# Kernel optimization log

Measured on AMD Instinct MI355X. Metric: run time of the kernel, lower is better.

The kernel has to match this reference:

```python
import jax, jax.numpy as jnp
import numpy as np

B, S, H = 2, 2048, 2048
NQ, NKV = 32, 8
HD = H // NQ  # 64


def setup_inputs() -> dict:
    key = jax.random.key(0)
    ks = jax.random.split(key, 9)
    s = 1.0 / np.sqrt(H)
    return {
        "x": jax.random.normal(ks[0], (B, S, H), dtype=jnp.float32),
        "Wq": jax.random.normal(ks[1], (H, H), dtype=jnp.float32) * s,
        "bq": jnp.zeros((H,), dtype=jnp.float32),
        "Wk": jax.random.normal(ks[2], (H, NKV * HD), dtype=jnp.float32) * s,
        "bk": jnp.zeros((NKV * HD,), dtype=jnp.float32),
        "Wv": jax.random.normal(ks[3], (H, NKV * HD), dtype=jnp.float32) * s,
        "bv": jnp.zeros((NKV * HD,), dtype=jnp.float32),
        "Wo": jax.random.normal(ks[4], (H, H), dtype=jnp.float32) * s,
        "bo": jnp.zeros((H,), dtype=jnp.float32),
    }


def reference(x, Wq, bq, Wk, bk, Wv, bv, Wo, bo):
    Bx, Sx, _ = x.shape
    g = NQ // NKV  # queries per kv head
    q = (x @ Wq + bq).reshape(Bx, Sx, NKV, g, HD)   # grouped query heads
    k = (x @ Wk + bk).reshape(Bx, Sx, NKV, HD)
    v = (x @ Wv + bv).reshape(Bx, Sx, NKV, HD)
    # scores: [B, NKV, g, S, S] -- broadcast KV across group instead of jnp.repeat
    scores = jnp.einsum('bshgd,bkhd->bhgsk', q, k) / jnp.sqrt(jnp.float32(HD))
    probs = jax.nn.softmax(scores, axis=-1)
    out = jnp.einsum('bhgsk,bkhd->bshgd', probs, v).reshape(Bx, Sx, H)
    return out @ Wo + bo
```

## Files before the change

### kernel.cpp

```cpp
#include <hip/hip_runtime.h>
#include <cstdint>
#include <cstddef>

typedef unsigned short u16;
typedef __bf16 bf16x8 __attribute__((ext_vector_type(8)));
typedef float f32x4 __attribute__((ext_vector_type(4)));
typedef unsigned short u16x4 __attribute__((ext_vector_type(4)));
typedef unsigned short u16x8 __attribute__((ext_vector_type(8)));
typedef uint32_t u32x4 __attribute__((ext_vector_type(4)));
typedef __attribute__((address_space(1))) unsigned int as1_uint;
typedef __attribute__((address_space(3))) unsigned int as3_uint;

__device__ __forceinline__ u16 f2bf(float f) {
  uint32_t u = __builtin_bit_cast(uint32_t, f);
  u += 0x7FFFu + ((u >> 16) & 1u);
  return (u16)(u >> 16);
}

__device__ __forceinline__ uint32_t cvtpk2bf(float a, float b) {
  uint32_t r;
  asm("v_cvt_pk_bf16_f32 %0, %1, %2" : "=v"(r) : "v"(a), "v"(b));
  return r;
}

__device__ __forceinline__ float max3f(float a, float b, float c) {
  return fmaxf(fmaxf(a, b), c);
}

__device__ __forceinline__ void gld_lds16(const void* g, void* l) {
  __builtin_amdgcn_global_load_lds((as1_uint*)g, (as3_uint*)l, 16, 0, 0);
}

__global__ __launch_bounds__(256) void k_cast(const float* __restrict__ in,
                                              u16* __restrict__ out, int n8) {
  int i = blockIdx.x * 256 + threadIdx.x;
  if (i >= n8) return;
  const float4* p = reinterpret_cast<const float4*>(in) + (size_t)i * 2;
  float4 a = p[0], b = p[1];
  u16x8 r;
  r[0] = f2bf(a.x); r[1] = f2bf(a.y); r[2] = f2bf(a.z); r[3] = f2bf(a.w);
  r[4] = f2bf(b.x); r[5] = f2bf(b.y); r[6] = f2bf(b.z); r[7] = f2bf(b.w);
  *reinterpret_cast<u16x8*>(out + (size_t)i * 8) = r;
}

__global__ __launch_bounds__(256) void k_transpose_all(const float* __restrict__ Wq,
                                                       const float* __restrict__ Wk,
                                                       const float* __restrict__ Wv,
                                                       const float* __restrict__ Wo,
                                                       u16* __restrict__ wqkvT,
                                                       u16* __restrict__ woT) {
  constexpr int K = 2048;
  const int z = blockIdx.z;
  const float* W; u16* Wt; int N;
  if (z == 0)      { W = Wq; Wt = wqkvT;                        N = 2048; }
  else if (z == 1) { W = Wo; Wt = woT;                          N = 2048; }
  else if (z == 2) { W = Wk; Wt = wqkvT + (size_t)2048 * 2048;  N = 512;  }
  else             { W = Wv; Wt = wqkvT + (size_t)2560 * 2048;  N = 512;  }
  const int n0 = blockIdx.x * 64;
  if (n0 >= N) return;
  __shared__ u16 tile[64][72];
  const int k0 = blockIdx.y * 64;
  const int r = threadIdx.x >> 4;
  const int c4 = (threadIdx.x & 15) * 4;
#pragma unroll
  for (int i = 0; i < 4; ++i) {
    int kk = r + i * 16;
    float4 v = *reinterpret_cast<const float4*>(W + (size_t)(k0 + kk) * N + n0 + c4);
    tile[kk][c4 + 0] = f2bf(v.x); tile[kk][c4 + 1] = f2bf(v.y);
    tile[kk][c4 + 2] = f2bf(v.z); tile[kk][c4 + 3] = f2bf(v.w);
  }
  __syncthreads();
#pragma unroll
  for (int i = 0; i < 4; ++i) {
    int nn = r + i * 16;
    u16x4 o;
    o[0] = tile[c4 + 0][nn]; o[1] = tile[c4 + 1][nn];
    o[2] = tile[c4 + 2][nn]; o[3] = tile[c4 + 3][nn];
    *reinterpret_cast<u16x4*>(Wt + (size_t)(n0 + nn) * K + k0 + c4) = o;
  }
}

__global__ __launch_bounds__(256) void k_transpose_v(const u16* __restrict__ qkv,
                                                     u16* __restrict__ vt) {
  __shared__ u16 tile[64][72];
  const int t0 = blockIdx.x * 64, kvh = blockIdx.y, b = blockIdx.z;
  const u16* src = qkv + ((size_t)(b * 2048) + t0) * 3072 + 2560 + kvh * 64;
  u16* dst = vt + ((size_t)(b * 8 + kvh) * 64) * 2048 + t0;
  const int r = threadIdx.x >> 3;
  const int c8 = (threadIdx.x & 7) * 8;
#pragma unroll
  for (int i = 0; i < 2; ++i) {
    int rr = r + i * 32;
    u16x8 v = *reinterpret_cast<const u16x8*>(src + (size_t)rr * 3072 + c8);
#pragma unroll
    for (int j = 0; j < 8; ++j) tile[c8 + j][rr] = v[j];
  }
  __syncthreads();
#pragma unroll
  for (int i = 0; i < 2; ++i) {
    int rr = r + i * 32;
    u16x8 o;
#pragma unroll
    for (int j = 0; j < 8; ++j) o[j] = tile[rr][c8 + j];
    *reinterpret_cast<u16x8*>(dst + (size_t)rr * 2048 + c8) = o;
  }
}

template <bool F32OUT>
__global__ __launch_bounds__(256) void k_gemm(const u16* __restrict__ A,
                                              const u16* __restrict__ Bt,
                                              const float* __restrict__ b0,
                                              const float* __restrict__ b1,
                                              const float* __restrict__ b2,
                                              void* __restrict__ Cout,
                                              int M, int N, int K,
                                              int n1, int n2,
                                              int scaleN, float scaleV) {
  __shared__ __align__(16) u16 As[128 * 64];
  __shared__ __align__(16) u16 Bs[128 * 64];
  const int id = blockIdx.y * gridDim.x + blockIdx.x;
  const int cpx = (gridDim.x * gridDim.y) >> 3;
  const int nid = (id & 7) * cpx + (id >> 3);
  const int m0 = (nid / gridDim.x) * 128, n0 = (nid % gridDim.x) * 128;
  const int tid = threadIdx.x;
  const int l = tid & 63, w = tid >> 6;
  const int wm = w >> 1, wn = w & 1;
  const int lr = l & 15, lo = l >> 4;
  const int srow = w * 8 + (l >> 3);
  const int sc = (l & 7) ^ ((l >> 3) & 7);
  f32x4 acc[4][4] = {};
  for (int kt = 0; kt < K; kt += 64) {
    __syncthreads();
#pragma unroll
    for (int it = 0; it < 4; ++it) {
      int row = it * 32 + srow;
      gld_lds16(A + (size_t)(m0 + row) * K + kt + sc * 8,
                (char*)As + (it * 32 + w * 8) * 128);
      gld_lds16(Bt + (size_t)(n0 + row) * K + kt + sc * 8,
                (char*)Bs + (it * 32 + w * 8) * 128);
    }
    __syncthreads();
    bf16x8 af[4][2], bfr[4][2];
#pragma unroll
    for (int mi = 0; mi < 4; ++mi) {
      int row = wm * 64 + mi * 16 + lr;
#pragma unroll
      for (int ks = 0; ks < 2; ++ks) {
        int ch = (ks * 4 + lo) ^ (row & 7);
        af[mi][ks] = *reinterpret_cast<const bf16x8*>((const char*)As + row * 128 + ch * 16);
      }
    }
#pragma unroll
    for (int nj = 0; nj < 4; ++nj) {
      int row = wn * 64 + nj * 16 + lr;
#pragma unroll
      for (int ks = 0; ks < 2; ++ks) {
        int ch = (ks * 4 + lo) ^ (row & 7);
        bfr[nj][ks] = *reinterpret_cast<const bf16x8*>((const char*)Bs + row * 128 + ch * 16);
      }
    }
#pragma unroll
    for (int mi = 0; mi < 4; ++mi)
#pragma unroll
      for (int nj = 0; nj < 4; ++nj) {
        acc[mi][nj] = __builtin_amdgcn_mfma_f32_16x16x32_bf16(af[mi][0], bfr[nj][0], acc[mi][nj], 0, 0, 0);
        acc[mi][nj] = __builtin_amdgcn_mfma_f32_16x16x32_bf16(af[mi][1], bfr[nj][1], acc[mi][nj], 0, 0, 0);
      }
  }
#pragma unroll
  for (int mi = 0; mi < 4; ++mi) {
    int row = m0 + wm * 64 + mi * 16 + lo * 4;
#pragma unroll
    for (int nj = 0; nj < 4; ++nj) {
      int col = n0 + wn * 64 + nj * 16 + lr;
      float bv = (col < n1) ? b0[col] : (col < n2 ? b1[col - n1] : b2[col - n2]);
      float scc = (col < scaleN) ? scaleV : 1.0f;
#pragma unroll
      for (int r = 0; r < 4; ++r) {
        float v = (acc[mi][nj][r] + bv) * scc;
        if (F32OUT) ((float*)Cout)[(size_t)(row + r) * N + col] = v;
        else        ((u16*)Cout)[(size_t)(row + r) * N + col] = f2bf(v);
      }
    }
  }
}

__global__ __launch_bounds__(256, 4) void k_attn(const u16* __restrict__ QKV,
                                                 const u16* __restrict__ VT,
                                                 u16* __restrict__ Oa) {
  constexpr int S = 2048, LDQ = 3072;
  constexpr float THR = 8.0f;
  __shared__ __align__(16) u16 Ks[2][64 * 64];
  __shared__ __align__(16) u16 Vs[2][64 * 64];
  const int qt = blockIdx.x, h = blockIdx.y, b = blockIdx.z;
  const int kvh = h >> 2;
  const int tid = threadIdx.x, l = tid & 63, w = tid >> 6;
  const int lr = l & 15, lo = l >> 4;
  const size_t base = (size_t)b * S * LDQ;
  const u16* Qg = QKV + base + h * 64;
  const u16* Kg = QKV + base + 2048 + kvh * 64;
  const u16* Vg = VT + (size_t)(b * 8 + kvh) * 64 * 2048;
  const int qrow = qt * 64 + w * 16 + lr;
  const bf16x8 aq0 = *reinterpret_cast<const bf16x8*>(Qg + (size_t)qrow * LDQ + lo * 8);
  const bf16x8 aq1 = *reinterpret_cast<const bf16x8*>(Qg + (size_t)qrow * LDQ + 32 + lo * 8);
  f32x4 acc[4] = {};
  float mrun = -1e30f, lsum = 0.f;
  const int krow = w * 8 + (l >> 3);
  const int ksc = (l & 7) ^ ((l >> 3) & 7);
  gld_lds16(Kg + (size_t)krow * LDQ + ksc * 8, (char*)Ks[0] + (w * 8) * 128);
  gld_lds16(Kg + (size_t)(32 + krow) * LDQ + ksc * 8, (char*)Ks[0] + (32 + w * 8) * 128);
  gld_lds16(Vg + (size_t)krow * 2048 + ksc * 8, (char*)Vs[0] + (w * 8) * 128);
  gld_lds16(Vg + (size_t)(32 + krow) * 2048 + ksc * 8, (char*)Vs[0] + (32 + w * 8) * 128);
  int cur = 0;
  for (int kt = 0; kt < S; kt += 64) {
    __syncthreads();
    if (kt + 64 < S) {
      const int nb = cur ^ 1, nk = kt + 64;
      gld_lds16(Kg + (size_t)(nk + krow) * LDQ + ksc * 8, (char*)Ks[nb] + (w * 8) * 128);
      gld_lds16(Kg + (size_t)(nk + 32 + krow) * LDQ + ksc * 8, (char*)Ks[nb] + (32 + w * 8) * 128);
      gld_lds16(Vg + (size_t)krow * 2048 + nk + ksc * 8, (char*)Vs[nb] + (w * 8) * 128);
      gld_lds16(Vg + (size_t)(32 + krow) * 2048 + nk + ksc * 8, (char*)Vs[nb] + (32 + w * 8) * 128);
    }
    float p[16];
    const u16* KsC = Ks[cur];
    __builtin_amdgcn_s_setprio(1);
#pragma unroll
    for (int t = 0; t < 4; ++t) {
      const int row = t * 16 + lr;
      bf16x8 k0 = *reinterpret_cast<const bf16x8*>((const char*)KsC + row * 128 + ((lo ^ (row & 7)) * 16));
      bf16x8 k1 = *reinterpret_cast<const bf16x8*>((const char*)KsC + row * 128 + (((4 + lo) ^ (row & 7)) * 16));
      f32x4 zz = {};
      zz = __builtin_amdgcn_mfma_f32_16x16x32_bf16(k0, aq0, zz, 0, 0, 0);
      zz = __builtin_amdgcn_mfma_f32_16x16x32_bf16(k1, aq1, zz, 0, 0, 0);
#pragma unroll
      for (int r = 0; r < 4; ++r) p[t * 4 + r] = zz[r];
    }
    __builtin_amdgcn_s_setprio(0);
    float m0 = max3f(p[0], p[1], p[2]);
    float m1 = max3f(p[3], p[4], p[5]);
    float m2 = max3f(p[6], p[7], p[8]);
    float m3 = max3f(p[9], p[10], p[11]);
    float m4 = max3f(p[12], p[13], p[14]);
    float tm = fmaxf(max3f(m0, m1, m2), max3f(m3, m4, p[15]));
    tm = fmaxf(tm, __shfl_xor(tm, 16, 64));
    tm = fmaxf(tm, __shfl_xor(tm, 32, 64));
    if (__all(tm <= mrun + THR)) {
#pragma unroll
      for (int i = 0; i < 16; ++i) p[i] = __builtin_amdgcn_exp2f(p[i] - mrun);
    } else {
      float mnew = fmaxf(mrun, tm);
      float alpha = __builtin_amdgcn_exp2f(mrun - mnew);
      mrun = mnew;
#pragma unroll
      for (int i = 0; i < 16; ++i) p[i] = __builtin_amdgcn_exp2f(p[i] - mnew);
      lsum *= alpha;
#pragma unroll
      for (int r = 0; r < 4; ++r) {
        float ar = __shfl(alpha, lo * 4 + r, 64);
#pragma unroll
        for (int nj = 0; nj < 4; ++nj) acc[nj][r] *= ar;
      }
    }
    float rs = (((p[0] + p[1]) + (p[2] + p[3])) + ((p[4] + p[5]) + (p[6] + p[7])))
             + (((p[8] + p[9]) + (p[10] + p[11])) + ((p[12] + p[13]) + (p[14] + p[15])));
    rs += __shfl_xor(rs, 16, 64);
    rs += __shfl_xor(rs, 32, 64);
    lsum += rs;
    uint32_t w00 = cvtpk2bf(p[0], p[1]),   w01 = cvtpk2bf(p[2], p[3]);
    uint32_t w10 = cvtpk2bf(p[4], p[5]),   w11 = cvtpk2bf(p[6], p[7]);
    uint32_t w20 = cvtpk2bf(p[8], p[9]),   w21 = cvtpk2bf(p[10], p[11]);
    uint32_t w30 = cvtpk2bf(p[12], p[13]), w31 = cvtpk2bf(p[14], p[15]);
    asm volatile("v_permlane32_swap_b32 %0, %1" : "+v"(w00), "+v"(w10));
    asm volatile("v_permlane16_swap_b32 %0, %1" : "+v"(w00), "+v"(w10));
    asm volatile("v_permlane32_swap_b32 %0, %1" : "+v"(w01), "+v"(w11));
    asm volatile("v_permlane16_swap_b32 %0, %1" : "+v"(w01), "+v"(w11));
    asm volatile("v_permlane32_swap_b32 %0, %1" : "+v"(w20), "+v"(w30));
    asm volatile("v_permlane16_swap_b32 %0, %1" : "+v"(w20), "+v"(w30));
    asm volatile("v_permlane32_swap_b32 %0, %1" : "+v"(w21), "+v"(w31));
    asm volatile("v_permlane16_swap_b32 %0, %1" : "+v"(w21), "+v"(w31));
    u32x4 pq0; pq0[0] = w00; pq0[1] = w01; pq0[2] = w10; pq0[3] = w11;
    u32x4 pq1; pq1[0] = w20; pq1[1] = w21; pq1[2] = w30; pq1[3] = w31;
    const bf16x8 pa0 = __builtin_bit_cast(bf16x8, pq0);
    const bf16x8 pa1 = __builtin_bit_cast(bf16x8, pq1);
    const u16* VsC = Vs[cur];
    __builtin_amdgcn_s_setprio(1);
#pragma unroll
    for (int nj = 0; nj < 4; ++nj) {
      const int vr = nj * 16 + lr;
      const bf16x8 bv0 = *reinterpret_cast<const bf16x8*>((const char*)VsC + vr * 128 + ((lo ^ (vr & 7)) * 16));
      const bf16x8 bv1 = *reinterpret_cast<const bf16x8*>((const char*)VsC + vr * 128 + (((4 + lo) ^ (vr & 7)) * 16));
      acc[nj] = __builtin_amdgcn_mfma_f32_16x16x32_bf16(pa0, bv0, acc[nj], 0, 0, 0);
      acc[nj] = __builtin_amdgcn_mfma_f32_16x16x32_bf16(pa1, bv1, acc[nj], 0, 0, 0);
    }
    __builtin_amdgcn_s_setprio(0);
    cur ^= 1;
  }
  float lf[4];
#pragma unroll
  for (int r = 0; r < 4; ++r) lf[r] = 1.0f / __shfl(lsum, lo * 4 + r, 64);
  const size_t orow = (size_t)b * S + qt * 64 + w * 16 + lo * 4;
#pragma unroll
  for (int nj = 0; nj < 4; ++nj) {
    const int col = h * 64 + nj * 16 + lr;
#pragma unroll
    for (int r = 0; r < 4; ++r)
      Oa[(orow + r) * 2048 + col] = f2bf(acc[nj][r] * lf[r]);
  }
}

extern "C" void kernel_launch(void* const* d_in, const int* in_sizes, int n_in,
                              void* d_out, int out_size, void* d_ws, size_t ws_size,
                              hipStream_t stream) {
  const float* x  = (const float*)d_in[0];
  const float* Wq = (const float*)d_in[1];
  const float* bq = (const float*)d_in[2];
  const float* Wk = (const float*)d_in[3];
  const float* bk = (const float*)d_in[4];
  const float* Wv = (const float*)d_in[5];
  const float* bv = (const float*)d_in[6];
  const float* Wo = (const float*)d_in[7];
  const float* bo = (const float*)d_in[8];
  float* out = (float*)d_out;
  char* ws = (char*)d_ws;

  u16*   xb    = (u16*)(ws + 0);
  u16*   vtg   = (u16*)(ws + 0);
  u16*   wqkvT = (u16*)(ws + 16777216);
  u16*   woT   = (u16*)(ws + 29360128);
  u16*   qkv   = (u16*)(ws + 37748736);
  u16*   attn  = (u16*)(ws + 62914560);

  const float SCL = 0.125f * 1.44269504088896341f;

  k_cast<<<4096, 256, 0, stream>>>(x, xb, 1048576);
  k_transpose_all<<<dim3(32, 32, 4), 256, 0, stream>>>(Wq, Wk, Wv, Wo, wqkvT, woT);
  k_gemm<false><<<dim3(24, 32), 256, 0, stream>>>(xb, wqkvT, bq, bk, bv, qkv,
                                                  4096, 3072, 2048, 2048, 2560, 2048, SCL);
  k_transpose_v<<<dim3(32, 8, 2), 256, 0, stream>>>(qkv, vtg);
  k_attn<<<dim3(32, 32, 2), 256, 0, stream>>>(qkv, vtg, attn);
  k_gemm<true><<<dim3(16, 32), 256, 0, stream>>>(attn, woT, bo, bo, bo, out,
                                                 4096, 2048, 2048, 2048, 4096, 0, 1.0f);
}
```

Measured before the change: 293.0 us.

## Enlarge attention query tile to 256 rows with 8 waves, two sub-tiles each

The attention kernel now gives each 512-thread block 256 query rows, with every wave handling two 16-row query sub-tiles. Each K/V tile loaded into shared memory is therefore reused by four times as many query rows, and every K and V register fragment feeds two MFMA chains. This cuts global-to-LDS traffic and LDS reads per unit of work and gives each wave more independent MFMA work. The cost is higher register pressure from two sets of accumulators, softmax state and P values per wave. The grid also shrinks to 512 blocks, which may reduce occupancy and balance across CUs.

```diff
diff --git a/kernel.cpp b/kernel.cpp
--- a/kernel.cpp
+++ b/kernel.cpp
@@ -185,11 +185,60 @@
   }
 }
 
-__global__ __launch_bounds__(256, 4) void k_attn(const u16* __restrict__ QKV,
+__device__ __forceinline__ void softmax_pack(float (&p)[16], float& mrun, float& lsum,
+                                             f32x4 (&acc)[4], int lo,
+                                             u32x4& pq0, u32x4& pq1) {
+  constexpr float THR = 8.0f;
+  float m0 = max3f(p[0], p[1], p[2]);
+  float m1 = max3f(p[3], p[4], p[5]);
+  float m2 = max3f(p[6], p[7], p[8]);
+  float m3 = max3f(p[9], p[10], p[11]);
+  float m4 = max3f(p[12], p[13], p[14]);
+  float tm = fmaxf(max3f(m0, m1, m2), max3f(m3, m4, p[15]));
+  tm = fmaxf(tm, __shfl_xor(tm, 16, 64));
+  tm = fmaxf(tm, __shfl_xor(tm, 32, 64));
+  if (__all(tm <= mrun + THR)) {
+#pragma unroll
+    for (int i = 0; i < 16; ++i) p[i] = __builtin_amdgcn_exp2f(p[i] - mrun);
+  } else {
+    float mnew = fmaxf(mrun, tm);
+    float alpha = __builtin_amdgcn_exp2f(mrun - mnew);
+    mrun = mnew;
+#pragma unroll
+    for (int i = 0; i < 16; ++i) p[i] = __builtin_amdgcn_exp2f(p[i] - mnew);
+    lsum *= alpha;
+#pragma unroll
+    for (int r = 0; r < 4; ++r) {
+      float ar = __shfl(alpha, lo * 4 + r, 64);
+#pragma unroll
+      for (int nj = 0; nj < 4; ++nj) acc[nj][r] *= ar;
+    }
+  }
+  float rs = (((p[0] + p[1]) + (p[2] + p[3])) + ((p[4] + p[5]) + (p[6] + p[7])))
+           + (((p[8] + p[9]) + (p[10] + p[11])) + ((p[12] + p[13]) + (p[14] + p[15])));
+  rs += __shfl_xor(rs, 16, 64);
+  rs += __shfl_xor(rs, 32, 64);
+  lsum += rs;
+  uint32_t w00 = cvtpk2bf(p[0], p[1]),   w01 = cvtpk2bf(p[2], p[3]);
+  uint32_t w10 = cvtpk2bf(p[4], p[5]),   w11 = cvtpk2bf(p[6], p[7]);
+  uint32_t w20 = cvtpk2bf(p[8], p[9]),   w21 = cvtpk2bf(p[10], p[11]);
+  uint32_t w30 = cvtpk2bf(p[12], p[13]), w31 = cvtpk2bf(p[14], p[15]);
+  asm volatile("v_permlane32_swap_b32 %0, %1" : "+v"(w00), "+v"(w10));
+  asm volatile("v_permlane16_swap_b32 %0, %1" : "+v"(w00), "+v"(w10));
+  asm volatile("v_permlane32_swap_b32 %0, %1" : "+v"(w01), "+v"(w11));
+  asm volatile("v_permlane16_swap_b32 %0, %1" : "+v"(w01), "+v"(w11));
+  asm volatile("v_permlane32_swap_b32 %0, %1" : "+v"(w20), "+v"(w30));
+  asm volatile("v_permlane16_swap_b32 %0, %1" : "+v"(w20), "+v"(w30));
+  asm volatile("v_permlane32_swap_b32 %0, %1" : "+v"(w21), "+v"(w31));
+  asm volatile("v_permlane16_swap_b32 %0, %1" : "+v"(w21), "+v"(w31));
+  pq0[0] = w00; pq0[1] = w01; pq0[2] = w10; pq0[3] = w11;
+  pq1[0] = w20; pq1[1] = w21; pq1[2] = w30; pq1[3] = w31;
+}
+
+__global__ __launch_bounds__(512, 4) void k_attn(const u16* __restrict__ QKV,
                                                  const u16* __restrict__ VT,
                                                  u16* __restrict__ Oa) {
   constexpr int S = 2048, LDQ = 3072;
-  constexpr float THR = 8.0f;
   __shared__ __align__(16) u16 Ks[2][64 * 64];
   __shared__ __align__(16) u16 Vs[2][64 * 64];
   const int qt = blockIdx.x, h = blockIdx.y, b = blockIdx.z;
@@ -200,28 +249,26 @@
   const u16* Qg = QKV + base + h * 64;
   const u16* Kg = QKV + base + 2048 + kvh * 64;
   const u16* Vg = VT + (size_t)(b * 8 + kvh) * 64 * 2048;
-  const int qrow = qt * 64 + w * 16 + lr;
-  const bf16x8 aq0 = *reinterpret_cast<const bf16x8*>(Qg + (size_t)qrow * LDQ + lo * 8);
-  const bf16x8 aq1 = *reinterpret_cast<const bf16x8*>(Qg + (size_t)qrow * LDQ + 32 + lo * 8);
-  f32x4 acc[4] = {};
-  float mrun = -1e30f, lsum = 0.f;
-  const int krow = w * 8 + (l >> 3);
+  const int qrow0 = qt * 256 + w * 32 + lr;
+  const bf16x8 aq0 = *reinterpret_cast<const bf16x8*>(Qg + (size_t)qrow0 * LDQ + lo * 8);
+  const bf16x8 aq1 = *reinterpret_cast<const bf16x8*>(Qg + (size_t)qrow0 * LDQ + 32 + lo * 8);
+  const bf16x8 aq2 = *reinterpret_cast<const bf16x8*>(Qg + (size_t)(qrow0 + 16) * LDQ + lo * 8);
+  const bf16x8 aq3 = *reinterpret_cast<const bf16x8*>(Qg + (size_t)(qrow0 + 16) * LDQ + 32 + lo * 8);
+  f32x4 acc0[4] = {}, acc1[4] = {};
+  float mrun0 = -1e30f, lsum0 = 0.f, mrun1 = -1e30f, lsum1 = 0.f;
+  const int krow = tid >> 3;
   const int ksc = (l & 7) ^ ((l >> 3) & 7);
   gld_lds16(Kg + (size_t)krow * LDQ + ksc * 8, (char*)Ks[0] + (w * 8) * 128);
-  gld_lds16(Kg + (size_t)(32 + krow) * LDQ + ksc * 8, (char*)Ks[0] + (32 + w * 8) * 128);
   gld_lds16(Vg + (size_t)krow * 2048 + ksc * 8, (char*)Vs[0] + (w * 8) * 128);
-  gld_lds16(Vg + (size_t)(32 + krow) * 2048 + ksc * 8, (char*)Vs[0] + (32 + w * 8) * 128);
   int cur = 0;
   for (int kt = 0; kt < S; kt += 64) {
     __syncthreads();
     if (kt + 64 < S) {
       const int nb = cur ^ 1, nk = kt + 64;
       gld_lds16(Kg + (size_t)(nk + krow) * LDQ + ksc * 8, (char*)Ks[nb] + (w * 8) * 128);
-      gld_lds16(Kg + (size_t)(nk + 32 + krow) * LDQ + ksc * 8, (char*)Ks[nb] + (32 + w * 8) * 128);
       gld_lds16(Vg + (size_t)krow * 2048 + nk + ksc * 8, (char*)Vs[nb] + (w * 8) * 128);
-      gld_lds16(Vg + (size_t)(32 + krow) * 2048 + nk + ksc * 8, (char*)Vs[nb] + (32 + w * 8) * 128);
-    }
-    float p[16];
+    }
+    float p0[16], p1[16];
     const u16* KsC = Ks[cur];
     __builtin_amdgcn_s_setprio(1);
 #pragma unroll
@@ -229,59 +276,22 @@
       const int row = t * 16 + lr;
       bf16x8 k0 = *reinterpret_cast<const bf16x8*>((const char*)KsC + row * 128 + ((lo ^ (row & 7)) * 16));
       bf16x8 k1 = *reinterpret_cast<const bf16x8*>((const char*)KsC + row * 128 + (((4 + lo) ^ (row & 7)) * 16));
-      f32x4 zz = {};
-      zz = __builtin_amdgcn_mfma_f32_16x16x32_bf16(k0, aq0, zz, 0, 0, 0);
-      zz = __builtin_amdgcn_mfma_f32_16x16x32_bf16(k1, aq1, zz, 0, 0, 0);
-#pragma unroll
-      for (int r = 0; r < 4; ++r) p[t * 4 + r] = zz[r];
+      f32x4 z0 = {}, z1 = {};
+      z0 = __builtin_amdgcn_mfma_f32_16x16x32_bf16(k0, aq0, z0, 0, 0, 0);
+      z0 = __builtin_amdgcn_mfma_f32_16x16x32_bf16(k1, aq1, z0, 0, 0, 0);
+      z1 = __builtin_amdgcn_mfma_f32_16x16x32_bf16(k0, aq2, z1, 0, 0, 0);
+      z1 = __builtin_amdgcn_mfma_f32_16x16x32_bf16(k1, aq3, z1, 0, 0, 0);
+#pragma unroll
+      for (int r = 0; r < 4; ++r) { p0[t * 4 + r] = z0[r]; p1[t * 4 + r] = z1[r]; }
     }
     __builtin_amdgcn_s_setprio(0);
-    float m0 = max3f(p[0], p[1], p[2]);
-    float m1 = max3f(p[3], p[4], p[5]);
-    float m2 = max3f(p[6], p[7], p[8]);
-    float m3 = max3f(p[9], p[10], p[11]);
-    float m4 = max3f(p[12], p[13], p[14]);
-    float tm = fmaxf(max3f(m0, m1, m2), max3f(m3, m4, p[15]));
-    tm = fmaxf(tm, __shfl_xor(tm, 16, 64));
-    tm = fmaxf(tm, __shfl_xor(tm, 32, 64));
-    if (__all(tm <= mrun + THR)) {
-#pragma unroll
-      for (int i = 0; i < 16; ++i) p[i] = __builtin_amdgcn_exp2f(p[i] - mrun);
-    } else {
-      float mnew = fmaxf(mrun, tm);
-      float alpha = __builtin_amdgcn_exp2f(mrun - mnew);
-      mrun = mnew;
-#pragma unroll
-      for (int i = 0; i < 16; ++i) p[i] = __builtin_amdgcn_exp2f(p[i] - mnew);
-      lsum *= alpha;
-#pragma unroll
-      for (int r = 0; r < 4; ++r) {
-        float ar = __shfl(alpha, lo * 4 + r, 64);
-#pragma unroll
-        for (int nj = 0; nj < 4; ++nj) acc[nj][r] *= ar;
-      }
-    }
-    float rs = (((p[0] + p[1]) + (p[2] + p[3])) + ((p[4] + p[5]) + (p[6] + p[7])))
-             + (((p[8] + p[9]) + (p[10] + p[11])) + ((p[12] + p[13]) + (p[14] + p[15])));
-    rs += __shfl_xor(rs, 16, 64);
-    rs += __shfl_xor(rs, 32, 64);
-    lsum += rs;
-    uint32_t w00 = cvtpk2bf(p[0], p[1]),   w01 = cvtpk2bf(p[2], p[3]);
-    uint32_t w10 = cvtpk2bf(p[4], p[5]),   w11 = cvtpk2bf(p[6], p[7]);
-    uint32_t w20 = cvtpk2bf(p[8], p[9]),   w21 = cvtpk2bf(p[10], p[11]);
-    uint32_t w30 = cvtpk2bf(p[12], p[13]), w31 = cvtpk2bf(p[14], p[15]);
-    asm volatile("v_permlane32_swap_b32 %0, %1" : "+v"(w00), "+v"(w10));
-    asm volatile("v_permlane16_swap_b32 %0, %1" : "+v"(w00), "+v"(w10));
-    asm volatile("v_permlane32_swap_b32 %0, %1" : "+v"(w01), "+v"(w11));
-    asm volatile("v_permlane16_swap_b32 %0, %1" : "+v"(w01), "+v"(w11));
-    asm volatile("v_permlane32_swap_b32 %0, %1" : "+v"(w20), "+v"(w30));
-    asm volatile("v_permlane16_swap_b32 %0, %1" : "+v"(w20), "+v"(w30));
-    asm volatile("v_permlane32_swap_b32 %0, %1" : "+v"(w21), "+v"(w31));
-    asm volatile("v_permlane16_swap_b32 %0, %1" : "+v"(w21), "+v"(w31));
-    u32x4 pq0; pq0[0] = w00; pq0[1] = w01; pq0[2] = w10; pq0[3] = w11;
-    u32x4 pq1; pq1[0] = w20; pq1[1] = w21; pq1[2] = w30; pq1[3] = w31;
+    u32x4 pq0, pq1, pq2, pq3;
+    softmax_pack(p0, mrun0, lsum0, acc0, lo, pq0, pq1);
+    softmax_pack(p1, mrun1, lsum1, acc1, lo, pq2, pq3);
     const bf16x8 pa0 = __builtin_bit_cast(bf16x8, pq0);
     const bf16x8 pa1 = __builtin_bit_cast(bf16x8, pq1);
+    const bf16x8 pa2 = __builtin_bit_cast(bf16x8, pq2);
+    const bf16x8 pa3 = __builtin_bit_cast(bf16x8, pq3);
     const u16* VsC = Vs[cur];
     __builtin_amdgcn_s_setprio(1);
 #pragma unroll
@@ -289,22 +299,29 @@
       const int vr = nj * 16 + lr;
       const bf16x8 bv0 = *reinterpret_cast<const bf16x8*>((const char*)VsC + vr * 128 + ((lo ^ (vr & 7)) * 16));
       const bf16x8 bv1 = *reinterpret_cast<const bf16x8*>((const char*)VsC + vr * 128 + (((4 + lo) ^ (vr & 7)) * 16));
-      acc[nj] = __builtin_amdgcn_mfma_f32_16x16x32_bf16(pa0, bv0, acc[nj], 0, 0, 0);
-      acc[nj] = __builtin_amdgcn_mfma_f32_16x16x32_bf16(pa1, bv1, acc[nj], 0, 0, 0);
+      acc0[nj] = __builtin_amdgcn_mfma_f32_16x16x32_bf16(pa0, bv0, acc0[nj], 0, 0, 0);
+      acc0[nj] = __builtin_amdgcn_mfma_f32_16x16x32_bf16(pa1, bv1, acc0[nj], 0, 0, 0);
+      acc1[nj] = __builtin_amdgcn_mfma_f32_16x16x32_bf16(pa2, bv0, acc1[nj], 0, 0, 0);
+      acc1[nj] = __builtin_amdgcn_mfma_f32_16x16x32_bf16(pa3, bv1, acc1[nj], 0, 0, 0);
     }
     __builtin_amdgcn_s_setprio(0);
     cur ^= 1;
   }
-  float lf[4];
-#pragma unroll
-  for (int r = 0; r < 4; ++r) lf[r] = 1.0f / __shfl(lsum, lo * 4 + r, 64);
-  const size_t orow = (size_t)b * S + qt * 64 + w * 16 + lo * 4;
+  float lf0[4], lf1[4];
+#pragma unroll
+  for (int r = 0; r < 4; ++r) {
+    lf0[r] = 1.0f / __shfl(lsum0, lo * 4 + r, 64);
+    lf1[r] = 1.0f / __shfl(lsum1, lo * 4 + r, 64);
+  }
+  const size_t orow0 = (size_t)b * S + qt * 256 + w * 32 + lo * 4;
 #pragma unroll
   for (int nj = 0; nj < 4; ++nj) {
     const int col = h * 64 + nj * 16 + lr;
 #pragma unroll
-    for (int r = 0; r < 4; ++r)
-      Oa[(orow + r) * 2048 + col] = f2bf(acc[nj][r] * lf[r]);
+    for (int r = 0; r < 4; ++r) {
+      Oa[(orow0 + r) * 2048 + col] = f2bf(acc0[nj][r] * lf0[r]);
+      Oa[(orow0 + 16 + r) * 2048 + col] = f2bf(acc1[nj][r] * lf1[r]);
+    }
   }
 }
 
@@ -337,7 +354,7 @@
   k_gemm<false><<<dim3(24, 32), 256, 0, stream>>>(xb, wqkvT, bq, bk, bv, qkv,
                                                   4096, 3072, 2048, 2048, 2560, 2048, SCL);
   k_transpose_v<<<dim3(32, 8, 2), 256, 0, stream>>>(qkv, vtg);
-  k_attn<<<dim3(32, 32, 2), 256, 0, stream>>>(qkv, vtg, attn);
+  k_attn<<<dim3(8, 32, 2), 512, 0, stream>>>(qkv, vtg, attn);
   k_gemm<true><<<dim3(16, 32), 256, 0, stream>>>(attn, woT, bo, bo, bo, out,
                                                  4096, 2048, 2048, 2048, 4096, 0, 1.0f);
 }
```

Result: no change. 288.8 us (-1.4%).
